# Optimization experiments

Hardware: AMD Instinct MI355X
Metric: run time of the kernel (lower is better)

## Reference

```python
import jax, jax.numpy as jnp
import numpy as np

OUT, IN, B = 11008, 4096, 32

def setup_inputs() -> dict:
    key = jax.random.key(0)
    k1, k2, k3, k4 = jax.random.split(key, 4)
    x = jax.random.normal(k1, (B, IN), dtype=jnp.float32)
    # ternary weights in {-1, 0, +1}, stored as int (int8 semantics)
    weight_q = jax.random.randint(k2, (OUT, IN), -1, 2, dtype=jnp.int32)
    # per-row positive scale (fp16 in torch, cast to fp32 at dequant time)
    weight_scale = jax.random.uniform(k3, (OUT, 1), dtype=jnp.float32, minval=0.01, maxval=1.0)
    bias = jax.random.normal(k4, (OUT,), dtype=jnp.float32)
    return {"x": x, "weight_q": weight_q, "weight_scale": weight_scale, "bias": bias}

def reference(x, weight_q, weight_scale, bias):
    # dequantize_2bit: int8 ternary * per-row scale -> fp32 weight [OUT, IN]
    W = weight_q.astype(jnp.float32) * weight_scale.astype(jnp.float32)
    # F.linear: x @ W.T + bias
    return jnp.einsum('bi,oi->bo', x.astype(jnp.float32), W) + bias
```

## Files before the change

kernel.cpp:

```cpp
#include <hip/hip_runtime.h>

#define OUT_N 11008
#define IN_K  4096
#define BATCH 32
#define SEGS  16
#define KSEG  (IN_K / SEGS)
#define OPB   64
#define WSTR  (KSEG + 8)

typedef __attribute__((ext_vector_type(8))) short short8;
typedef __attribute__((ext_vector_type(4))) float float4v;

__global__ __launch_bounds__(256) void init_kernel(
    const float* __restrict__ bias, float* __restrict__ out)
{
    int i = blockIdx.x * 256 + threadIdx.x;
    if (i < BATCH * OUT_N) out[i] = bias[i % OUT_N];
}

__device__ __forceinline__ unsigned short f2bf(float f) {
    unsigned u = __builtin_bit_cast(unsigned, f);
    unsigned r = u + 0x7FFFu + ((u >> 16) & 1u);
    return (unsigned short)(r >> 16);
}

__device__ __forceinline__ unsigned pkbf16(float fhi, float flo) {
    return __builtin_amdgcn_perm(__builtin_bit_cast(unsigned, fhi),
                                 __builtin_bit_cast(unsigned, flo),
                                 0x07060302u);
}

__global__ __launch_bounds__(256, 2) void lin2bit_kernel(
    const int* __restrict__ wq, const float* __restrict__ scale,
    const float* __restrict__ x, float* __restrict__ out)
{
    __shared__ unsigned short wl[OPB][WSTR];
    __shared__ unsigned short xs[BATCH][WSTR];

    const int t    = threadIdx.x;
    const int lane = t & 63;
    const int wave = t >> 6;
    const int kseg = blockIdx.y * KSEG;
    const int o0   = blockIdx.x * OPB;

#pragma unroll
    for (int it = 0; it < 8; ++it) {
        int idx = it * 256 + t;
        int b   = idx >> 6;
        int k4  = idx & 63;
        float4 v = *reinterpret_cast<const float4*>(x + b * IN_K + kseg + k4 * 4);
        ushort4 h = { f2bf(v.x), f2bf(v.y), f2bf(v.z), f2bf(v.w) };
        *reinterpret_cast<ushort4*>(&xs[b][k4 * 4]) = h;
    }

#pragma unroll
    for (int r = 0; r < 16; ++r) {
        const int rl = wave * 16 + r;
        const int4 v = *reinterpret_cast<const int4*>(
            wq + (size_t)(o0 + rl) * IN_K + kseg + lane * 4);
        unsigned lo = pkbf16((float)v.y, (float)v.x);
        unsigned hi = pkbf16((float)v.w, (float)v.z);
        uint2 p = { lo, hi };
        *reinterpret_cast<uint2*>(&wl[rl][lane * 4]) = p;
    }
    __syncthreads();

    const int quad = lane >> 4;
    const int l16  = lane & 15;
    const int o    = o0 + wave * 16 + l16;

    const unsigned short* wrow = &wl[wave * 16 + l16][quad * 8];
    const unsigned short* xrow0 = &xs[l16][quad * 8];
    const unsigned short* xrow1 = &xs[l16 + 16][quad * 8];

    float4v acc0 = {0.f, 0.f, 0.f, 0.f};
    float4v acc1 = {0.f, 0.f, 0.f, 0.f};

#pragma unroll
    for (int kt = 0; kt < KSEG / 32; ++kt) {
        short8 bfrag = *reinterpret_cast<const short8*>(wrow + kt * 32);
        short8 a0    = *reinterpret_cast<const short8*>(xrow0 + kt * 32);
        short8 a1    = *reinterpret_cast<const short8*>(xrow1 + kt * 32);
        acc0 = __builtin_amdgcn_mfma_f32_16x16x32_bf16(a0, bfrag, acc0, 0, 0, 0);
        acc1 = __builtin_amdgcn_mfma_f32_16x16x32_bf16(a1, bfrag, acc1, 0, 0, 0);
    }

    const float s = scale[o];
    const int b0 = quad * 4;
#pragma unroll
    for (int r = 0; r < 4; ++r) {
        unsafeAtomicAdd(out + (size_t)(b0 + r)      * OUT_N + o, s * acc0[r]);
        unsafeAtomicAdd(out + (size_t)(b0 + r + 16) * OUT_N + o, s * acc1[r]);
    }
}

extern "C" void kernel_launch(void* const* d_in, const int* in_sizes, int n_in,
                              void* d_out, int out_size, void* d_ws, size_t ws_size,
                              hipStream_t stream) {
    const float* x     = (const float*)d_in[0];
    const int*   wq    = (const int*)d_in[1];
    const float* scale = (const float*)d_in[2];
    const float* bias  = (const float*)d_in[3];
    float* out = (float*)d_out;

    init_kernel<<<dim3((BATCH * OUT_N + 255) / 256), 256, 0, stream>>>(bias, out);
    lin2bit_kernel<<<dim3(OUT_N / OPB, SEGS), 256, 0, stream>>>(wq, scale, x, out);
}
```

Before: 255.8 us.

## Pipeline weight loads over K chunks with double-buffered LDS, halve K-split

The kernel's K range per block doubles (SEGS 16 to 8), and the weight tile is streamed in 64-wide chunks. Chunks go through a double-buffered LDS tile, with register prefetch of the next chunk overlapping the MFMA work on the current one. This is meant to hide global load latency, cut LDS footprint for weights, and halve the number of atomic adds to the output. The costs are a __syncthreads per chunk, a longer serial loop per block, fewer blocks in the grid, and a larger per-block x tile.

New measurement: 268.4 us. 1.05x slower.

```diff
diff --git a/kernel.cpp b/kernel.cpp
--- a/kernel.cpp
+++ b/kernel.cpp
@@ -3,10 +3,13 @@
 #define OUT_N 11008
 #define IN_K  4096
 #define BATCH 32
-#define SEGS  16
+#define SEGS  8
 #define KSEG  (IN_K / SEGS)
+#define CK    64
+#define NCH   (KSEG / CK)
 #define OPB   64
-#define WSTR  (KSEG + 8)
+#define XSTR  516
+#define WSTR  68
 
 typedef __attribute__((ext_vector_type(8))) short short8;
 typedef __attribute__((ext_vector_type(4))) float float4v;
@@ -30,12 +33,12 @@
                                  0x07060302u);
 }
 
-__global__ __launch_bounds__(256, 2) void lin2bit_kernel(
+__global__ __launch_bounds__(256, 3) void lin2bit_kernel(
     const int* __restrict__ wq, const float* __restrict__ scale,
     const float* __restrict__ x, float* __restrict__ out)
 {
-    __shared__ unsigned short wl[OPB][WSTR];
-    __shared__ unsigned short xs[BATCH][WSTR];
+    __shared__ unsigned short xs[BATCH][XSTR];
+    __shared__ unsigned short wl[2][OPB][WSTR];
 
     const int t    = threadIdx.x;
     const int lane = t & 63;
@@ -44,46 +47,75 @@
     const int o0   = blockIdx.x * OPB;
 
 #pragma unroll
-    for (int it = 0; it < 8; ++it) {
+    for (int it = 0; it < 16; ++it) {
         int idx = it * 256 + t;
-        int b   = idx >> 6;
-        int k4  = idx & 63;
+        int b   = idx >> 7;
+        int k4  = idx & 127;
         float4 v = *reinterpret_cast<const float4*>(x + b * IN_K + kseg + k4 * 4);
         ushort4 h = { f2bf(v.x), f2bf(v.y), f2bf(v.z), f2bf(v.w) };
         *reinterpret_cast<ushort4*>(&xs[b][k4 * 4]) = h;
     }
 
-#pragma unroll
-    for (int r = 0; r < 16; ++r) {
-        const int rl = wave * 16 + r;
-        const int4 v = *reinterpret_cast<const int4*>(
-            wq + (size_t)(o0 + rl) * IN_K + kseg + lane * 4);
-        unsigned lo = pkbf16((float)v.y, (float)v.x);
-        unsigned hi = pkbf16((float)v.w, (float)v.z);
-        uint2 p = { lo, hi };
-        *reinterpret_cast<uint2*>(&wl[rl][lane * 4]) = p;
-    }
+    const int rsub = lane >> 4;
+    const int csub = lane & 15;
+    const int* __restrict__ wbase =
+        wq + (size_t)(o0 + wave * 16 + rsub) * IN_K + kseg + csub * 4;
+
+#define WLOAD(c, r)                                                           \
+    do {                                                                      \
+        _Pragma("unroll")                                                     \
+        for (int j = 0; j < 4; ++j)                                           \
+            (r)[j] = *reinterpret_cast<const int4*>(                          \
+                wbase + (size_t)(j * 4) * IN_K + (c) * CK);                   \
+    } while (0)
+
+#define WSTORE(c, r)                                                          \
+    do {                                                                      \
+        _Pragma("unroll")                                                     \
+        for (int j = 0; j < 4; ++j) {                                         \
+            unsigned lo = pkbf16((float)(r)[j].y, (float)(r)[j].x);           \
+            unsigned hi = pkbf16((float)(r)[j].w, (float)(r)[j].z);           \
+            uint2 p = { lo, hi };                                             \
+            *reinterpret_cast<uint2*>(                                        \
+                &wl[(c) & 1][wave * 16 + j * 4 + rsub][csub * 4]) = p;        \
+        }                                                                     \
+    } while (0)
+
+    int4 cur[4], nxt[4];
+    WLOAD(0, cur);
+    WSTORE(0, cur);
+    WLOAD(1, nxt);
     __syncthreads();
 
     const int quad = lane >> 4;
     const int l16  = lane & 15;
     const int o    = o0 + wave * 16 + l16;
 
-    const unsigned short* wrow = &wl[wave * 16 + l16][quad * 8];
-    const unsigned short* xrow0 = &xs[l16][quad * 8];
-    const unsigned short* xrow1 = &xs[l16 + 16][quad * 8];
-
     float4v acc0 = {0.f, 0.f, 0.f, 0.f};
     float4v acc1 = {0.f, 0.f, 0.f, 0.f};
 
+    for (int c = 0; c < NCH; ++c) {
+        const unsigned short* wrow = &wl[c & 1][wave * 16 + l16][quad * 8];
+        const unsigned short* x0   = &xs[l16][c * CK + quad * 8];
+        const unsigned short* x1   = &xs[l16 + 16][c * CK + quad * 8];
 #pragma unroll
-    for (int kt = 0; kt < KSEG / 32; ++kt) {
-        short8 bfrag = *reinterpret_cast<const short8*>(wrow + kt * 32);
-        short8 a0    = *reinterpret_cast<const short8*>(xrow0 + kt * 32);
-        short8 a1    = *reinterpret_cast<const short8*>(xrow1 + kt * 32);
-        acc0 = __builtin_amdgcn_mfma_f32_16x16x32_bf16(a0, bfrag, acc0, 0, 0, 0);
-        acc1 = __builtin_amdgcn_mfma_f32_16x16x32_bf16(a1, bfrag, acc1, 0, 0, 0);
+        for (int kt = 0; kt < CK / 32; ++kt) {
+            short8 bfrag = *reinterpret_cast<const short8*>(wrow + kt * 32);
+            short8 a0    = *reinterpret_cast<const short8*>(x0 + kt * 32);
+            short8 a1    = *reinterpret_cast<const short8*>(x1 + kt * 32);
+            acc0 = __builtin_amdgcn_mfma_f32_16x16x32_bf16(a0, bfrag, acc0, 0, 0, 0);
+            acc1 = __builtin_amdgcn_mfma_f32_16x16x32_bf16(a1, bfrag, acc1, 0, 0, 0);
+        }
+        if (c + 1 < NCH) {
+#pragma unroll
+            for (int j = 0; j < 4; ++j) cur[j] = nxt[j];
+            WSTORE(c + 1, cur);
+            if (c + 2 < NCH) WLOAD(c + 2, nxt);
+        }
+        __syncthreads();
     }
+#undef WLOAD
+#undef WSTORE
 
     const float s = scale[o];
     const int b0 = quad * 4;
```
